# Performance work log

Measured on AMD Instinct MI355X. Metric: run time of the kernel, lower is better.

The kernel has to match this reference:

```python
import jax, jax.numpy as jnp
import numpy as np

H, DM, N, K, R = 768, 1536, 16, 4, 48  # hidden, intermediate, state, conv kernel, dt rank
B, L = 2, 1024


def _silu(x):
    return x * jax.nn.sigmoid(x)


def _causal_conv(x, w, b):
    # x: [B, D, L]; w: [D, K] depthwise; causal left-pad K-1 (matches causal_conv1d_fn)
    out = jax.lax.conv_general_dilated(
        x, w[:, None, :], window_strides=(1,), padding=[(K - 1, 0)],
        feature_group_count=w.shape[0], dimension_numbers=('NCH', 'OIH', 'NCH'))
    return out + b[None, :, None]


def _selective_scan(u, delta, A, Bm, Cm, Dp, gate):
    # u/delta/gate: [B, D, L]; A: [D, N]; Bm/Cm: [B, L, N]; Dp: [D]
    dA = jnp.exp(delta[:, :, :, None] * A[None, :, None, :])              # [B,D,L,N]
    dBu = delta[:, :, :, None] * Bm[:, None, :, :] * u[:, :, :, None]      # [B,D,L,N]
    dA_t = jnp.moveaxis(dA, 2, 0)    # [L,B,D,N]
    dBu_t = jnp.moveaxis(dBu, 2, 0)  # [L,B,D,N]
    C_t = jnp.moveaxis(Cm, 1, 0)     # [L,B,N]

    def step(x, inp):
        a, bu, c = inp
        x = a * x + bu                               # [B,D,N]
        y = jnp.einsum('bdn,bn->bd', x, c)
        return x, y

    x0 = jnp.zeros(dA_t.shape[1:], dA_t.dtype)
    _, ys = jax.lax.scan(step, x0, (dA_t, dBu_t, C_t))
    y = jnp.moveaxis(ys, 0, 2) + u * Dp[None, :, None]   # [B,D,L]
    return y * _silu(gate)


def _branch(conv_out, gate, xw, dtw, dtb, Alog, Dp):
    # conv_out/gate: [B, D, L]
    ssm = jnp.einsum('bdl,pd->blp', conv_out, xw)        # [B,L,R+2N]
    ts, Bm, Cm = ssm[..., :R], ssm[..., R:R + N], ssm[..., R + N:]
    delta = jax.nn.softplus(jnp.einsum('dr,blr->bdl', dtw, ts) + dtb[None, :, None])
    A = -jnp.exp(Alog)
    return _selective_scan(conv_out, delta, A, Bm, Cm, Dp, gate)


def setup_inputs() -> dict:
    key = jax.random.key(0)
    ks = jax.random.split(key, 12)
    s = 0.02
    hidden_states = jax.random.normal(ks[0], (B, L, H), jnp.float32)
    in_proj_w = jax.random.normal(ks[1], (2 * DM, H), jnp.float32) * s
    conv_w = jax.random.normal(ks[2], (DM, K), jnp.float32) * 0.3
    conv_b = jax.random.normal(ks[3], (DM,), jnp.float32) * s
    x_proj_w = jax.random.normal(ks[4], (R + 2 * N, DM), jnp.float32) * s
    dt_proj_w = jax.random.normal(ks[5], (DM, R), jnp.float32) * s
    dt_proj_b = -4.0 + 0.1 * jax.random.normal(ks[6], (DM,), jnp.float32)
    x_proj_back_w = jax.random.normal(ks[7], (R + 2 * N, DM), jnp.float32) * s
    dt_proj_back_w = jax.random.normal(ks[8], (DM, R), jnp.float32) * s
    dt_proj_back_b = -4.0 + 0.1 * jax.random.normal(ks[9], (DM,), jnp.float32)
    A_log = jnp.log(jnp.broadcast_to(jnp.arange(1, N + 1, dtype=jnp.float32)[None, :], (DM, N)))
    A_log_back = A_log
    D = jnp.ones((DM,), jnp.float32)
    D_back = jnp.ones((DM,), jnp.float32)
    out_proj_w = jax.random.normal(ks[10], (H, DM), jnp.float32) * s
    return {
        'hidden_states': hidden_states, 'in_proj_w': in_proj_w,
        'conv_w': conv_w, 'conv_b': conv_b,
        'x_proj_w': x_proj_w, 'dt_proj_w': dt_proj_w, 'dt_proj_b': dt_proj_b,
        'x_proj_back_w': x_proj_back_w, 'dt_proj_back_w': dt_proj_back_w,
        'dt_proj_back_b': dt_proj_back_b, 'A_log': A_log, 'A_log_back': A_log_back,
        'D': D, 'D_back': D_back, 'out_proj_w': out_proj_w,
    }


def reference(hidden_states, in_proj_w, conv_w, conv_b, x_proj_w, dt_proj_w,
              dt_proj_b, x_proj_back_w, dt_proj_back_w, dt_proj_back_b,
              A_log, A_log_back, D, D_back, out_proj_w):
    proj = jnp.einsum('blh,ph->bpl', hidden_states, in_proj_w)  # [B,2D,L]
    x, gate = proj[:, :DM], proj[:, DM:]
    conv_out = _silu(_causal_conv(x, conv_w, conv_b))           # [B,D,L]
    # forward-direction scan
    y_f = _branch(conv_out, gate, x_proj_w, dt_proj_w, dt_proj_b, A_log, D)
    # backward-direction scan on time-flipped conv output and gate
    y_b = _branch(conv_out[:, :, ::-1], gate[:, :, ::-1], x_proj_back_w,
                  dt_proj_back_w, dt_proj_back_b, A_log_back, D_back)
    y = y_f + y_b[:, :, ::-1]
    return jnp.einsum('bdl,hd->blh', y, out_proj_w)
```

## Files before the change

### kernel.cpp

```cpp
#include <hip/hip_runtime.h>
#include <math.h>

constexpr int cH  = 768;
constexpr int cDM = 1536;
constexpr int cN  = 16;
constexpr int cR  = 48;
constexpr int cB  = 2;
constexpr int cL  = 1024;
constexpr int cPS = 160;
constexpr int cCK = 32;

typedef unsigned short u16;
typedef __attribute__((ext_vector_type(8))) short bf16x8;
typedef __attribute__((ext_vector_type(4))) float f32x4;

__device__ __forceinline__ u16 f2bf(float f) {
    unsigned u = __float_as_uint(f);
    u += 0x7FFF + ((u >> 16) & 1);
    return (u16)(u >> 16);
}
__device__ __forceinline__ float bf2f(u16 h) {
    return __uint_as_float((unsigned)h << 16);
}
__device__ __forceinline__ float fexp2(float x) {
    float r; asm("v_exp_f32 %0, %1" : "=v"(r) : "v"(x)); return r;
}
constexpr float cLOG2E = 1.44269504f;

__global__ __launch_bounds__(256)
void prep_kernel(const float* __restrict__ hid, const float* __restrict__ inw,
                 const float* __restrict__ xpw, const float* __restrict__ xpbw,
                 const float* __restrict__ outw, const float* __restrict__ dtw,
                 const float* __restrict__ dtbw,
                 u16* __restrict__ hid_b, u16* __restrict__ inw_b,
                 u16* __restrict__ xpw2_b, u16* __restrict__ outw_b,
                 u16* __restrict__ dtw2_b)
{
    const long i8 = ((long)blockIdx.x * 256 + threadIdx.x) * 8;
    const long e0 = 1572864;
    const long e1 = e0 + 2359296;
    const long e2 = e1 + 122880;
    const long e3 = e2 + 122880;
    const long e4 = e3 + 1179648;
    const long e5 = e4 + 98304;
    const long e6 = e5 + 98304;
    const float* in; u16* out; long off; int pad = 0;
    if      (i8 < e0) { in = hid;  out = hid_b;           off = i8; }
    else if (i8 < e1) { in = inw;  out = inw_b;           off = i8 - e0; }
    else if (i8 < e2) { in = xpw;  out = xpw2_b;          off = i8 - e1; }
    else if (i8 < e3) { in = xpbw; out = xpw2_b + 122880; off = i8 - e2; }
    else if (i8 < e4) { in = outw; out = outw_b;          off = i8 - e3; }
    else if (i8 < e5) { in = dtw;  out = dtw2_b;          off = i8 - e4; pad = 1; }
    else if (i8 < e6) { in = dtbw; out = dtw2_b + 98304;  off = i8 - e5; pad = 1; }
    else return;
    u16 o[8];
    if (!pad) {
        const float4 a = *(const float4*)&in[off];
        const float4 b = *(const float4*)&in[off + 4];
        o[0]=f2bf(a.x); o[1]=f2bf(a.y); o[2]=f2bf(a.z); o[3]=f2bf(a.w);
        o[4]=f2bf(b.x); o[5]=f2bf(b.y); o[6]=f2bf(b.z); o[7]=f2bf(b.w);
    } else {
        const long r = off >> 6; const int k0 = (int)(off & 63);
        #pragma unroll
        for (int k = 0; k < 8; ++k)
            o[k] = (k0 + k < cR) ? f2bf(in[r * cR + k0 + k]) : (u16)0;
    }
    *(uint4*)&out[off] = *(uint4*)o;
}

__global__ __launch_bounds__(256)
void tspad_kernel(const float* __restrict__ ssms, u16* __restrict__ out) {
    int i = blockIdx.x * 256 + threadIdx.x;
    int dirsel = i >> 17;
    int rem = i & 131071;
    int bl = rem >> 6, k = rem & 63;
    out[i] = (k < cR) ? f2bf(ssms[(long)bl * cPS + dirsel * 80 + k]) : (u16)0;
}

__global__ __launch_bounds__(256)
void comb_kernel(u16* __restrict__ yf, const u16* __restrict__ yb, long n8) {
    long i = (long)blockIdx.x * 256 + threadIdx.x;
    if (i >= n8) return;
    uint4 av = ((uint4*)yf)[i];
    uint4 bv = ((const uint4*)yb)[i];
    unsigned* ap = (unsigned*)&av;
    unsigned* bp = (unsigned*)&bv;
    #pragma unroll
    for (int j = 0; j < 4; ++j) {
        const float lo = bf2f((u16)(ap[j] & 0xffff)) + bf2f((u16)(bp[j] & 0xffff));
        const float hi = bf2f((u16)(ap[j] >> 16))    + bf2f((u16)(bp[j] >> 16));
        ap[j] = (unsigned)f2bf(lo) | ((unsigned)f2bf(hi) << 16);
    }
    ((uint4*)yf)[i] = av;
}

__device__ __forceinline__ void gld_lds16(const u16* g, u16* l) {
    __builtin_amdgcn_global_load_lds(
        (const __attribute__((address_space(1))) unsigned int*)g,
        (__attribute__((address_space(3))) unsigned int*)l, 16, 0, 0);
}

#define GST(SA, SB, k0) do {                                                   \
    _Pragma("unroll")                                                          \
    for (int h = 0; h < 3; ++h) {                                              \
        const int q  = wid * 3 + h;                                            \
        const int rw = lane >> 2;                                              \
        if (q < 4) {                                                           \
            const int r  = q * 16 + rw;                                        \
            const int sw = (r & 3) ^ ((r >> 2) & 3);                           \
            const int kg = (k0) + (((lane & 3) ^ sw) << 3);                    \
            gld_lds16(Ab + (long)(m0 + r) * lda + kg, &SA[q * 512]);           \
        } else {                                                               \
            const int r  = (q - 4) * 16 + rw;                                  \
            const int sw = (r & 3) ^ ((r >> 2) & 3);                           \
            const int kg = (k0) + (((lane & 3) ^ sw) << 3);                    \
            int nr = n0 + r; if (nr > N2 - 1) nr = N2 - 1;                     \
            gld_lds16(Bb + (long)nr * ldb + kg, &SB[(q - 4) * 512]);           \
        }                                                                      \
    }                                                                          \
} while (0)

#define CMP(SA, SB) do {                                                       \
    bf16x8 af[4], bfr[2];                                                      \
    _Pragma("unroll")                                                          \
    for (int i = 0; i < 4; ++i) {                                              \
        const int ra  = i * 16 + lr;                                           \
        const int swa = (ra & 3) ^ ((ra >> 2) & 3);                            \
        af[i] = *(const bf16x8*)&SA[ra * 32 + ((lc ^ swa) << 3)];              \
    }                                                                          \
    _Pragma("unroll")                                                          \
    for (int j = 0; j < 2; ++j) {                                              \
        const int rb  = wn + j * 16 + lr;                                      \
        const int swb = (rb & 3) ^ ((rb >> 2) & 3);                            \
        bfr[j] = *(const bf16x8*)&SB[rb * 32 + ((lc ^ swb) << 3)];             \
    }                                                                          \
    _Pragma("unroll")                                                          \
    for (int i = 0; i < 4; ++i)                                                \
        _Pragma("unroll")                                                      \
        for (int j = 0; j < 2; ++j)                                            \
            acc[i][j] = __builtin_amdgcn_mfma_f32_16x16x32_bf16(af[i], bfr[j], acc[i][j], 0, 0, 0); \
} while (0)

template<int EPI>
__global__ __launch_bounds__(256, 4)
void gemm_mfma(const u16* __restrict__ A, const u16* __restrict__ B,
               float* __restrict__ C0, float* __restrict__ C1,
               const float* __restrict__ bias,
               int N2, int Kd, int lda, int ldb, int ldc,
               long sA, long sC, int splitCol, int kspl)
{
    __shared__ __align__(16) u16 shA0[2048];
    __shared__ __align__(16) u16 shA1[2048];
    __shared__ __align__(16) u16 shB0[4096];
    __shared__ __align__(16) u16 shB1[4096];
    const int tid  = threadIdx.x;
    const int wid  = tid >> 6, lane = tid & 63;
    const int lr   = lane & 15, lc = lane >> 4;
    const int z    = blockIdx.z;
    const int bz   = z / kspl, ks = z % kspl;
    const int kpc  = Kd / kspl;
    const int kbeg = ks * kpc;
    const int nt   = kpc / 32;
    const int n0 = blockIdx.x * 128, m0 = blockIdx.y * 64;
    const int wn = wid * 32;

    const u16* Ab = A + (long)bz * sA;
    const u16* Bb = B;

    f32x4 acc[4][2] = {};

    GST(shA0, shB0, kbeg);
    __syncthreads();
    int t = 0;
    for (;;) {
        if (t + 1 < nt) GST(shA1, shB1, kbeg + (t + 1) * 32);
        CMP(shA0, shB0);
        __syncthreads();
        if (++t >= nt) break;
        if (t + 1 < nt) GST(shA0, shB0, kbeg + (t + 1) * 32);
        CMP(shA1, shB1);
        __syncthreads();
        if (++t >= nt) break;
    }

    #pragma unroll
    for (int i = 0; i < 4; ++i) {
        #pragma unroll
        for (int e = 0; e < 4; ++e) {
            const int m = m0 + i * 16 + lc * 4 + e;
            float* base0 = C0 + (long)bz * sC + (long)m * ldc;
            float* base1 = (C1 != nullptr) ? C1 + (long)bz * sC + (long)m * ldc : nullptr;
            #pragma unroll
            for (int j = 0; j < 2; ++j) {
                const int n = n0 + wn + j * 16 + lr;
                if (n < N2) {
                    float v = acc[i][j][e];
                    if (EPI == 4) {
                        if (n < splitCol) base0[n] = v;
                        else base1[n - splitCol] = v / (1.f + __expf(-v));
                    } else if (EPI == 1) {
                        const float t2 = v + bias[n];
                        base0[n] = fmaxf(t2, 0.f) + __logf(1.f + __expf(-fabsf(t2)));
                    } else {
                        atomicAdd(base0 + n, v);
                    }
                }
            }
        }
    }
}

__global__ __launch_bounds__(256)
void conv_silu2(const float* __restrict__ x, const float* __restrict__ cw,
                const float* __restrict__ cb,
                float* __restrict__ convTf, u16* __restrict__ convT_b)
{
    __shared__ float xt[35][64];
    const int l0 = blockIdx.x * 32, d0 = blockIdx.y * 64, b = blockIdx.z;
    const int tid = threadIdx.x;
    for (int i = tid; i < 35 * 64; i += 256) {
        const int r = i >> 6, c = i & 63;
        const int l = l0 - 3 + r;
        xt[r][c] = (l >= 0) ? x[((long)b * cL + l) * cDM + d0 + c] : 0.f;
    }
    __syncthreads();
    const int dc = tid & 63, lsub = tid >> 6;
    const int d = d0 + dc;
    const float w0 = cw[d*4], w1 = cw[d*4+1], w2 = cw[d*4+2], w3 = cw[d*4+3];
    const float bi = cb[d];
    #pragma unroll
    for (int k = 0; k < 8; ++k) {
        const int row = lsub * 8 + k;
        float v = bi;
        v = fmaf(w0, xt[row][dc],     v);
        v = fmaf(w1, xt[row + 1][dc], v);
        v = fmaf(w2, xt[row + 2][dc], v);
        v = fmaf(w3, xt[row + 3][dc], v);
        const float s = v / (1.f + __expf(-v));
        const long o = ((long)b * cL + l0 + row) * cDM + d;
        convTf[o] = s;
        convT_b[o] = f2bf(s);
    }
}

#define SA_LOAD(g, DU, UU) _Pragma("unroll")                                   \
    for (int k = 0; k < 4; ++k) {                                              \
        const int t_ = (g) * 4 + k;                                            \
        const int l_ = dir ? (base - t_) : (base + t_);                        \
        const long off_ = (long)l_ * cDM + d;                                  \
        DU[k] = dT[off_]; UU[k] = uT[off_];                                    \
    }

#define SA_COMP(g, DU, UU) _Pragma("unroll")                                   \
    for (int k = 0; k < 4; ++k) {                                              \
        const int t_ = (g) * 4 + k;                                            \
        const float du_ = DU[k]; const float duu_ = du_ * UU[k];               \
        sdu += du_;                                                            \
        const float4 b0_ = *(const float4*)&bca[t_][half * 8];                 \
        const float4 b1_ = *(const float4*)&bca[t_][half * 8 + 4];             \
        const float bb_[8] = {b0_.x,b0_.y,b0_.z,b0_.w,b1_.x,b1_.y,b1_.z,b1_.w};\
        _Pragma("unroll")                                                      \
        for (int n = 0; n < 8; ++n)                                            \
            xs[n] = fmaf(fexp2(du_ * a2[n]), xs[n], duu_ * bb_[n]);            \
    }

__global__ __launch_bounds__(256, 4)
void scanA_kernel(const float* __restrict__ dT0, const float* __restrict__ dT1,
                  const float* __restrict__ uF, const float* __restrict__ ssms,
                  const float* __restrict__ AlogF, const float* __restrict__ AlogB,
                  float* __restrict__ Ap_out, float* __restrict__ Xf_out)
{
    __shared__ float bcA[4][32][16];
    const int tid = threadIdx.x;
    const int w = tid >> 6, lane = tid & 63;
    const int dd = lane & 31, half = lane >> 5;
    const int d = blockIdx.x * 32 + dd;
    const int b = blockIdx.y;
    const int zs = blockIdx.z * 4 + w;
    const int dir = zs >> 5, ck = zs & 31;
    const float* Alog = dir ? AlogB : AlogF;
    const float* dT = (dir ? dT1 : dT0) + (long)b * cL * cDM;
    const float* uT = uF + (long)b * cL * cDM;
    const float* sp = ssms + (long)b * cL * cPS;
    const int sofs = dir ? 128 : 48;
    const int base = dir ? (cL - 1 - ck * 32) : (ck * 32);
    float (*bca)[16] = bcA[w];

    #pragma unroll
    for (int h = 0; h < 2; ++h) {
        const int idx = h * 64 + lane;
        const int r = idx >> 2, q = idx & 3;
        const int lr_ = dir ? (base - r) : (base + r);
        *(float4*)&bca[r][q * 4] = *(const float4*)&sp[(long)lr_ * cPS + sofs + q * 4];
    }
    float a2[8];
    {
        const float4 a0 = *(const float4*)&Alog[d * 16 + half * 8];
        const float4 a1 = *(const float4*)&Alog[d * 16 + half * 8 + 4];
        a2[0]=-__expf(a0.x)*cLOG2E; a2[1]=-__expf(a0.y)*cLOG2E;
        a2[2]=-__expf(a0.z)*cLOG2E; a2[3]=-__expf(a0.w)*cLOG2E;
        a2[4]=-__expf(a1.x)*cLOG2E; a2[5]=-__expf(a1.y)*cLOG2E;
        a2[6]=-__expf(a1.z)*cLOG2E; a2[7]=-__expf(a1.w)*cLOG2E;
    }

    float xs[8] = {};
    float sdu = 0.f;

    float dX[4], uX[4], dY[4], uY[4], dZ[4], uZ[4];
    SA_LOAD(0, dX, uX);
    SA_LOAD(1, dY, uY);
    SA_LOAD(2, dZ, uZ);
    SA_COMP(0, dX, uX); SA_LOAD(3, dX, uX);
    SA_COMP(1, dY, uY); SA_LOAD(4, dY, uY);
    SA_COMP(2, dZ, uZ); SA_LOAD(5, dZ, uZ);
    SA_COMP(3, dX, uX); SA_LOAD(6, dX, uX);
    SA_COMP(4, dY, uY); SA_LOAD(7, dY, uY);
    SA_COMP(5, dZ, uZ);
    SA_COMP(6, dX, uX);
    SA_COMP(7, dY, uY);

    const long ob = (((long)(b * 2 + dir) * cCK + ck) * cDM + d) * 16 + half * 8;
    *(float4*)&Ap_out[ob]     = make_float4(fexp2(sdu*a2[0]), fexp2(sdu*a2[1]),
                                            fexp2(sdu*a2[2]), fexp2(sdu*a2[3]));
    *(float4*)&Ap_out[ob + 4] = make_float4(fexp2(sdu*a2[4]), fexp2(sdu*a2[5]),
                                            fexp2(sdu*a2[6]), fexp2(sdu*a2[7]));
    *(float4*)&Xf_out[ob]     = make_float4(xs[0], xs[1], xs[2], xs[3]);
    *(float4*)&Xf_out[ob + 4] = make_float4(xs[4], xs[5], xs[6], xs[7]);
}

__global__ __launch_bounds__(256)
void scanB_kernel(float* __restrict__ Ap, const float* __restrict__ Xf)
{
    const int gid = blockIdx.x * 256 + threadIdx.x;
    const int n = gid & 15;
    const int rest = gid >> 4;
    const int d = rest % cDM;
    const int b2 = rest / cDM;
    float x0 = 0.f;
    #pragma unroll
    for (int c = 0; c < cCK; ++c) {
        const long idx = (((long)b2 * cCK + c) * cDM + d) * 16 + n;
        const float ap = Ap[idx], xf = Xf[idx];
        Ap[idx] = x0;
        x0 = fmaf(ap, x0, xf);
    }
}

#define SC_LOAD(g, DU, UU, SG) _Pragma("unroll")                               \
    for (int k = 0; k < 4; ++k) {                                              \
        const int t_ = (g) * 4 + k;                                            \
        const int l_ = dir ? (base - t_) : (base + t_);                        \
        const long off_ = (long)l_ * cDM + d;                                  \
        DU[k] = dT[off_]; UU[k] = uT[off_];                                    \
        if (half == 0) SG[k] = sgp[off_];                                      \
    }

#define SC_COMP(g, DU, UU, SG) _Pragma("unroll")                               \
    for (int k = 0; k < 4; ++k) {                                              \
        const int t_ = (g) * 4 + k;                                            \
        const float du_ = DU[k]; const float uu_ = UU[k];                      \
        const float duu_ = du_ * uu_;                                          \
        const float4 b0_ = *(const float4*)&bcc[t_][half * 8];                 \
        const float4 b1_ = *(const float4*)&bcc[t_][half * 8 + 4];             \
        const float4 c0_ = *(const float4*)&bcc[t_][16 + half * 8];            \
        const float4 c1_ = *(const float4*)&bcc[t_][16 + half * 8 + 4];        \
        const float bb_[8] = {b0_.x,b0_.y,b0_.z,b0_.w,b1_.x,b1_.y,b1_.z,b1_.w};\
        const float cc_[8] = {c0_.x,c0_.y,c0_.z,c0_.w,c1_.x,c1_.y,c1_.z,c1_.w};\
        float y_ = 0.f;                                                        \
        _Pragma("unroll")                                                      \
        for (int n = 0; n < 8; ++n) {                                          \
            xs[n] = fmaf(fexp2(du_ * a2[n]), xs[n], duu_ * bb_[n]);            \
            y_ = fmaf(xs[n], cc_[n], y_);                                      \
        }                                                                      \
        y_ += __shfl_xor(y_, 32);                                              \
        if (half == 0) {                                                       \
            const int l2_ = dir ? (base - t_) : (base + t_);                   \
            const float val_ = (y_ + uu_ * Dd) * SG[k];                        \
            yout[((long)b * cL + l2_) * cDM + d] = f2bf(val_);                 \
        }                                                                      \
    }

__global__ __launch_bounds__(256, 4)
void scanC_kernel(const float* __restrict__ dT0, const float* __restrict__ dT1,
                  const float* __restrict__ uF, const float* __restrict__ sgF,
                  const float* __restrict__ ssms,
                  const float* __restrict__ AlogF, const float* __restrict__ AlogB,
                  const float* __restrict__ Df, const float* __restrict__ Db,
                  const float* __restrict__ X0,
                  u16* __restrict__ yf, u16* __restrict__ yb)
{
    __shared__ float bcS[4][32][32];
    const int tid = threadIdx.x;
    const int w = tid >> 6, lane = tid & 63;
    const int dd = lane & 31, half = lane >> 5;
    const int d = blockIdx.x * 32 + dd;
    const int b = blockIdx.y;
    const int zs = blockIdx.z * 4 + w;
    const int dir = zs >> 5, ck = zs & 31;
    const float* Alog = dir ? AlogB : AlogF;
    const float* dT = (dir ? dT1 : dT0) + (long)b * cL * cDM;
    const float* uT = uF + (long)b * cL * cDM;
    const float* sgp = sgF + (long)b * cL * cDM;
    const float* sp = ssms + (long)b * cL * cPS;
    const float Dd = dir ? Db[d] : Df[d];
    u16* yout = dir ? yb : yf;
    const int sofs = dir ? 128 : 48;
    const int base = dir ? (cL - 1 - ck * 32) : (ck * 32);
    float (*bcc)[32] = bcS[w];

    #pragma unroll
    for (int h = 0; h < 4; ++h) {
        const int idx = h * 64 + lane;
        const int r = idx >> 3, q = idx & 7;
        const int lr_ = dir ? (base - r) : (base + r);
        *(float4*)&bcc[r][q * 4] = *(const float4*)&sp[(long)lr_ * cPS + sofs + q * 4];
    }
    float a2[8];
    {
        const float4 a0 = *(const float4*)&Alog[d * 16 + half * 8];
        const float4 a1 = *(const float4*)&Alog[d * 16 + half * 8 + 4];
        a2[0]=-__expf(a0.x)*cLOG2E; a2[1]=-__expf(a0.y)*cLOG2E;
        a2[2]=-__expf(a0.z)*cLOG2E; a2[3]=-__expf(a0.w)*cLOG2E;
        a2[4]=-__expf(a1.x)*cLOG2E; a2[5]=-__expf(a1.y)*cLOG2E;
        a2[6]=-__expf(a1.z)*cLOG2E; a2[7]=-__expf(a1.w)*cLOG2E;
    }
    float xs[8];
    {
        const long ob = (((long)(b * 2 + dir) * cCK + ck) * cDM + d) * 16 + half * 8;
        const float4 x0v = *(const float4*)&X0[ob];
        const float4 x1v = *(const float4*)&X0[ob + 4];
        xs[0]=x0v.x; xs[1]=x0v.y; xs[2]=x0v.z; xs[3]=x0v.w;
        xs[4]=x1v.x; xs[5]=x1v.y; xs[6]=x1v.z; xs[7]=x1v.w;
    }

    float dX[4], uX[4], gX[4], dY[4], uY[4], gY[4], dZ[4], uZ[4], gZ[4];
    SC_LOAD(0, dX, uX, gX);
    SC_LOAD(1, dY, uY, gY);
    SC_LOAD(2, dZ, uZ, gZ);
    SC_COMP(0, dX, uX, gX); SC_LOAD(3, dX, uX, gX);
    SC_COMP(1, dY, uY, gY); SC_LOAD(4, dY, uY, gY);
    SC_COMP(2, dZ, uZ, gZ); SC_LOAD(5, dZ, uZ, gZ);
    SC_COMP(3, dX, uX, gX); SC_LOAD(6, dX, uX, gX);
    SC_COMP(4, dY, uY, gY); SC_LOAD(7, dY, uY, gY);
    SC_COMP(5, dZ, uZ, gZ);
    SC_COMP(6, dX, uX, gX);
    SC_COMP(7, dY, uY, gY);
}

extern "C" void kernel_launch(void* const* d_in, const int* in_sizes, int n_in,
                              void* d_out, int out_size, void* d_ws, size_t ws_size,
                              hipStream_t stream)
{
    const float* hid   = (const float*)d_in[0];
    const float* inw   = (const float*)d_in[1];
    const float* convw = (const float*)d_in[2];
    const float* convb = (const float*)d_in[3];
    const float* xpw   = (const float*)d_in[4];
    const float* dtw   = (const float*)d_in[5];
    const float* dtb   = (const float*)d_in[6];
    const float* xpbw  = (const float*)d_in[7];
    const float* dtbw  = (const float*)d_in[8];
    const float* dtbb  = (const float*)d_in[9];
    const float* Alog  = (const float*)d_in[10];
    const float* Alogb = (const float*)d_in[11];
    const float* Dv    = (const float*)d_in[12];
    const float* Dbv   = (const float*)d_in[13];
    const float* outw  = (const float*)d_in[14];
    float* out = (float*)d_out;

    float* ws = (float*)d_ws;
    const long S = (long)cB * cDM * cL;
    const long nSum = (long)2 * cB * cCK * cDM * 16;
    float* xbuf   = ws;
    float* sg     = ws + S;
    float* convTf = ws + 2 * S;
    float* deltaT1= ws + 3 * S;
    float* ssms   = ws + 4 * S;
    float* sumAp  = ssms + (long)cB * cL * cPS;
    float* sumXf  = sumAp + nSum;
    u16* ub       = (u16*)(sumXf + nSum);
    u16* convT_b  = ub;
    u16* yf_b     = convT_b + S;
    u16* yb_b     = yf_b + S;
    u16* ts2_b    = yb_b + S;
    u16* xpw2_b   = ts2_b + (long)2 * cB * cL * 64;
    u16* dtw2_b   = xpw2_b + (long)cPS * cDM;
    u16* outw_b   = dtw2_b + (long)2 * cDM * 64;
    u16* inw_b    = outw_b + (long)cH * cDM;
    u16* hid_b    = inw_b + (long)2 * cDM * cH;

    const dim3 blk(256);

    prep_kernel<<<dim3(2713), blk, 0, stream>>>(
        hid, inw, xpw, xpbw, outw, dtw, dtbw,
        hid_b, inw_b, xpw2_b, outw_b, dtw2_b);

    hipMemsetAsync(ssms, 0, (long)cB * cL * cPS * sizeof(float), stream);
    hipMemsetAsync(out, 0, (long)out_size * sizeof(float), stream);

    gemm_mfma<4><<<dim3(24, 16, cB), blk, 0, stream>>>(
        hid_b, inw_b, xbuf, sg, nullptr,
        2 * cDM, cH, cH, cH, cDM, (long)cL * cH, (long)cL * cDM, cDM, 1);

    conv_silu2<<<dim3(32, 24, cB), blk, 0, stream>>>(
        xbuf, convw, convb, convTf, convT_b);

    gemm_mfma<2><<<dim3(2, 16, cB * 8), blk, 0, stream>>>(
        convT_b, xpw2_b, ssms, nullptr, nullptr,
        cPS, cDM, cDM, cDM, cPS, (long)cL * cDM, (long)cL * cPS, 1 << 30, 8);

    tspad_kernel<<<1024, blk, 0, stream>>>(ssms, ts2_b);

    gemm_mfma<1><<<dim3(12, 16, cB), blk, 0, stream>>>(
        ts2_b, dtw2_b, xbuf, nullptr, dtb,
        cDM, 64, 64, 64, cDM, (long)cL * 64, (long)cL * cDM, 1 << 30, 1);
    gemm_mfma<1><<<dim3(12, 16, cB), blk, 0, stream>>>(
        ts2_b + (long)2 * cL * 64, dtw2_b + (long)cDM * 64, deltaT1, nullptr, dtbb,
        cDM, 64, 64, 64, cDM, (long)cL * 64, (long)cL * cDM, 1 << 30, 1);

    scanA_kernel<<<dim3(48, cB, 16), blk, 0, stream>>>(
        xbuf, deltaT1, convTf, ssms, Alog, Alogb, sumAp, sumXf);
    scanB_kernel<<<dim3(384), blk, 0, stream>>>(sumAp, sumXf);
    scanC_kernel<<<dim3(48, cB, 16), blk, 0, stream>>>(
        xbuf, deltaT1, convTf, sg, ssms, Alog, Alogb, Dv, Dbv,
        sumAp , yf_b, yb_b);

    comb_kernel<<<(int)(S / 8 / 256), blk, 0, stream>>>(yf_b, yb_b, S / 8);

    gemm_mfma<2><<<dim3(6, 16, cB * 2), blk, 0, stream>>>(
        yf_b, outw_b, out, nullptr, nullptr,
        cH, cDM, cDM, cDM, cH, (long)cL * cDM, (long)cL * cH, 1 << 30, 2);
}
```

Baseline: 169.1 us.

## Split scan kernels into single-wave blocks and store chunk delta sums instead of decay products

The scanA and scanC kernels are relaunched with one 64-thread wave per block instead of four waves sharing a block, which gives finer scheduling granularity and adds a __syncthreads after the shared B/C staging. ScanA now writes only the per-chunk sum of delta per channel rather than 16 exponentiated decay products, and scanB recomputes exp2(A*sum) itself. This cuts scanA output traffic, and scanB now writes the carried prefix state in place into the Xf buffer. The compute loops are also wrapped in s_setprio raises so the arithmetic phases get wave priority over loads.

```diff
diff --git a/kernel.cpp b/kernel.cpp
--- a/kernel.cpp
+++ b/kernel.cpp
@@ -251,47 +251,49 @@
         DU[k] = dT[off_]; UU[k] = uT[off_];                                    \
     }
 
-#define SA_COMP(g, DU, UU) _Pragma("unroll")                                   \
+#define SA_COMP(g, DU, UU) do {                                                \
+    __builtin_amdgcn_s_setprio(1);                                             \
+    _Pragma("unroll")                                                          \
     for (int k = 0; k < 4; ++k) {                                              \
         const int t_ = (g) * 4 + k;                                            \
         const float du_ = DU[k]; const float duu_ = du_ * UU[k];               \
         sdu += du_;                                                            \
-        const float4 b0_ = *(const float4*)&bca[t_][half * 8];                 \
-        const float4 b1_ = *(const float4*)&bca[t_][half * 8 + 4];             \
+        const float4 b0_ = *(const float4*)&bcA[t_][half * 8];                 \
+        const float4 b1_ = *(const float4*)&bcA[t_][half * 8 + 4];             \
         const float bb_[8] = {b0_.x,b0_.y,b0_.z,b0_.w,b1_.x,b1_.y,b1_.z,b1_.w};\
         _Pragma("unroll")                                                      \
         for (int n = 0; n < 8; ++n)                                            \
             xs[n] = fmaf(fexp2(du_ * a2[n]), xs[n], duu_ * bb_[n]);            \
-    }
-
-__global__ __launch_bounds__(256, 4)
+    }                                                                          \
+    __builtin_amdgcn_s_setprio(0);                                             \
+} while (0)
+
+__global__ __launch_bounds__(64, 4)
 void scanA_kernel(const float* __restrict__ dT0, const float* __restrict__ dT1,
                   const float* __restrict__ uF, const float* __restrict__ ssms,
                   const float* __restrict__ AlogF, const float* __restrict__ AlogB,
-                  float* __restrict__ Ap_out, float* __restrict__ Xf_out)
-{
-    __shared__ float bcA[4][32][16];
-    const int tid = threadIdx.x;
-    const int w = tid >> 6, lane = tid & 63;
+                  float* __restrict__ sdu_out, float* __restrict__ Xf_out)
+{
+    __shared__ float bcA[32][16];
+    const int lane = threadIdx.x;
     const int dd = lane & 31, half = lane >> 5;
     const int d = blockIdx.x * 32 + dd;
     const int b = blockIdx.y;
-    const int zs = blockIdx.z * 4 + w;
-    const int dir = zs >> 5, ck = zs & 31;
+    const int z = blockIdx.z;
+    const int dir = z >> 5, ck = z & 31;
     const float* Alog = dir ? AlogB : AlogF;
     const float* dT = (dir ? dT1 : dT0) + (long)b * cL * cDM;
     const float* uT = uF + (long)b * cL * cDM;
     const float* sp = ssms + (long)b * cL * cPS;
     const int sofs = dir ? 128 : 48;
     const int base = dir ? (cL - 1 - ck * 32) : (ck * 32);
-    float (*bca)[16] = bcA[w];
 
     #pragma unroll
     for (int h = 0; h < 2; ++h) {
         const int idx = h * 64 + lane;
         const int r = idx >> 2, q = idx & 3;
         const int lr_ = dir ? (base - r) : (base + r);
-        *(float4*)&bca[r][q * 4] = *(const float4*)&sp[(long)lr_ * cPS + sofs + q * 4];
+        *(float4*)&bcA[r][q * 4] = *(const float4*)&sp[(long)lr_ * cPS + sofs + q * 4];
     }
     float a2[8];
     {
@@ -302,6 +304,7 @@
         a2[4]=-__expf(a1.x)*cLOG2E; a2[5]=-__expf(a1.y)*cLOG2E;
         a2[6]=-__expf(a1.z)*cLOG2E; a2[7]=-__expf(a1.w)*cLOG2E;
     }
+    __syncthreads();
 
     float xs[8] = {};
     float sdu = 0.f;
@@ -319,29 +322,33 @@
     SA_COMP(6, dX, uX);
     SA_COMP(7, dY, uY);
 
+    if (half == 0)
+        sdu_out[((long)(b * 2 + dir) * cCK + ck) * cDM + d] = sdu;
     const long ob = (((long)(b * 2 + dir) * cCK + ck) * cDM + d) * 16 + half * 8;
-    *(float4*)&Ap_out[ob]     = make_float4(fexp2(sdu*a2[0]), fexp2(sdu*a2[1]),
-                                            fexp2(sdu*a2[2]), fexp2(sdu*a2[3]));
-    *(float4*)&Ap_out[ob + 4] = make_float4(fexp2(sdu*a2[4]), fexp2(sdu*a2[5]),
-                                            fexp2(sdu*a2[6]), fexp2(sdu*a2[7]));
     *(float4*)&Xf_out[ob]     = make_float4(xs[0], xs[1], xs[2], xs[3]);
     *(float4*)&Xf_out[ob + 4] = make_float4(xs[4], xs[5], xs[6], xs[7]);
 }
 
 __global__ __launch_bounds__(256)
-void scanB_kernel(float* __restrict__ Ap, const float* __restrict__ Xf)
+void scanB_kernel(const float* __restrict__ AlogF, const float* __restrict__ AlogB,
+                  const float* __restrict__ sduB, float* __restrict__ Xf)
 {
     const int gid = blockIdx.x * 256 + threadIdx.x;
     const int n = gid & 15;
     const int rest = gid >> 4;
     const int d = rest % cDM;
     const int b2 = rest / cDM;
+    const int dir = b2 & 1;
+    const float* Alog = dir ? AlogB : AlogF;
+    const float a2 = -__expf(Alog[d * 16 + n]) * cLOG2E;
     float x0 = 0.f;
     #pragma unroll
     for (int c = 0; c < cCK; ++c) {
-        const long idx = (((long)b2 * cCK + c) * cDM + d) * 16 + n;
-        const float ap = Ap[idx], xf = Xf[idx];
-        Ap[idx] = x0;
+        const long sidx = ((long)b2 * cCK + c) * cDM + d;
+        const float ap = fexp2(a2 * sduB[sidx]);
+        const long idx = sidx * 16 + n;
+        const float xf = Xf[idx];
+        Xf[idx] = x0;
         x0 = fmaf(ap, x0, xf);
     }
 }
@@ -355,15 +362,17 @@
         if (half == 0) SG[k] = sgp[off_];                                      \
     }
 
-#define SC_COMP(g, DU, UU, SG) _Pragma("unroll")                               \
+#define SC_COMP(g, DU, UU, SG) do {                                            \
+    __builtin_amdgcn_s_setprio(1);                                             \
+    _Pragma("unroll")                                                          \
     for (int k = 0; k < 4; ++k) {                                              \
         const int t_ = (g) * 4 + k;                                            \
         const float du_ = DU[k]; const float uu_ = UU[k];                      \
         const float duu_ = du_ * uu_;                                          \
-        const float4 b0_ = *(const float4*)&bcc[t_][half * 8];                 \
-        const float4 b1_ = *(const float4*)&bcc[t_][half * 8 + 4];             \
-        const float4 c0_ = *(const float4*)&bcc[t_][16 + half * 8];            \
-        const float4 c1_ = *(const float4*)&bcc[t_][16 + half * 8 + 4];        \
+        const float4 b0_ = *(const float4*)&bc[t_][half * 8];                  \
+        const float4 b1_ = *(const float4*)&bc[t_][half * 8 + 4];              \
+        const float4 c0_ = *(const float4*)&bc[t_][16 + half * 8];             \
+        const float4 c1_ = *(const float4*)&bc[t_][16 + half * 8 + 4];         \
         const float bb_[8] = {b0_.x,b0_.y,b0_.z,b0_.w,b1_.x,b1_.y,b1_.z,b1_.w};\
         const float cc_[8] = {c0_.x,c0_.y,c0_.z,c0_.w,c1_.x,c1_.y,c1_.z,c1_.w};\
         float y_ = 0.f;                                                        \
@@ -378,9 +387,11 @@
             const float val_ = (y_ + uu_ * Dd) * SG[k];                        \
             yout[((long)b * cL + l2_) * cDM + d] = f2bf(val_);                 \
         }                                                                      \
-    }
-
-__global__ __launch_bounds__(256, 4)
+    }                                                                          \
+    __builtin_amdgcn_s_setprio(0);                                             \
+} while (0)
+
+__global__ __launch_bounds__(64, 4)
 void scanC_kernel(const float* __restrict__ dT0, const float* __restrict__ dT1,
                   const float* __restrict__ uF, const float* __restrict__ sgF,
                   const float* __restrict__ ssms,
@@ -389,14 +400,13 @@
                   const float* __restrict__ X0,
                   u16* __restrict__ yf, u16* __restrict__ yb)
 {
-    __shared__ float bcS[4][32][32];
-    const int tid = threadIdx.x;
-    const int w = tid >> 6, lane = tid & 63;
+    __shared__ float bc[32][32];
+    const int lane = threadIdx.x;
     const int dd = lane & 31, half = lane >> 5;
     const int d = blockIdx.x * 32 + dd;
     const int b = blockIdx.y;
-    const int zs = blockIdx.z * 4 + w;
-    const int dir = zs >> 5, ck = zs & 31;
+    const int z = blockIdx.z;
+    const int dir = z >> 5, ck = z & 31;
     const float* Alog = dir ? AlogB : AlogF;
     const float* dT = (dir ? dT1 : dT0) + (long)b * cL * cDM;
     const float* uT = uF + (long)b * cL * cDM;
@@ -406,14 +416,13 @@
     u16* yout = dir ? yb : yf;
     const int sofs = dir ? 128 : 48;
     const int base = dir ? (cL - 1 - ck * 32) : (ck * 32);
-    float (*bcc)[32] = bcS[w];
 
     #pragma unroll
     for (int h = 0; h < 4; ++h) {
         const int idx = h * 64 + lane;
         const int r = idx >> 3, q = idx & 7;
         const int lr_ = dir ? (base - r) : (base + r);
-        *(float4*)&bcc[r][q * 4] = *(const float4*)&sp[(long)lr_ * cPS + sofs + q * 4];
+        *(float4*)&bc[r][q * 4] = *(const float4*)&sp[(long)lr_ * cPS + sofs + q * 4];
     }
     float a2[8];
     {
@@ -432,6 +441,7 @@
         xs[0]=x0v.x; xs[1]=x0v.y; xs[2]=x0v.z; xs[3]=x0v.w;
         xs[4]=x1v.x; xs[5]=x1v.y; xs[6]=x1v.z; xs[7]=x1v.w;
     }
+    __syncthreads();
 
     float dX[4], uX[4], gX[4], dY[4], uY[4], gY[4], dZ[4], uZ[4], gZ[4];
     SC_LOAD(0, dX, uX, gX);
@@ -471,14 +481,15 @@
     float* ws = (float*)d_ws;
     const long S = (long)cB * cDM * cL;
     const long nSum = (long)2 * cB * cCK * cDM * 16;
+    const long nSdu = (long)2 * cB * cCK * cDM;
     float* xbuf   = ws;
     float* sg     = ws + S;
     float* convTf = ws + 2 * S;
     float* deltaT1= ws + 3 * S;
     float* ssms   = ws + 4 * S;
-    float* sumAp  = ssms + (long)cB * cL * cPS;
-    float* sumXf  = sumAp + nSum;
-    u16* ub       = (u16*)(sumXf + nSum);
+    float* sumXf  = ssms + (long)cB * cL * cPS;
+    float* sduBuf = sumXf + nSum;
+    u16* ub       = (u16*)(sduBuf + nSdu);
     u16* convT_b  = ub;
     u16* yf_b     = convT_b + S;
     u16* yb_b     = yf_b + S;
@@ -518,12 +529,12 @@
         ts2_b + (long)2 * cL * 64, dtw2_b + (long)cDM * 64, deltaT1, nullptr, dtbb,
         cDM, 64, 64, 64, cDM, (long)cL * 64, (long)cL * cDM, 1 << 30, 1);
 
-    scanA_kernel<<<dim3(48, cB, 16), blk, 0, stream>>>(
-        xbuf, deltaT1, convTf, ssms, Alog, Alogb, sumAp, sumXf);
-    scanB_kernel<<<dim3(384), blk, 0, stream>>>(sumAp, sumXf);
-    scanC_kernel<<<dim3(48, cB, 16), blk, 0, stream>>>(
+    scanA_kernel<<<dim3(48, cB, 64), dim3(64), 0, stream>>>(
+        xbuf, deltaT1, convTf, ssms, Alog, Alogb, sduBuf, sumXf);
+    scanB_kernel<<<dim3(384), blk, 0, stream>>>(Alog, Alogb, sduBuf, sumXf);
+    scanC_kernel<<<dim3(48, cB, 64), dim3(64), 0, stream>>>(
         xbuf, deltaT1, convTf, sg, ssms, Alog, Alogb, Dv, Dbv,
-        sumAp , yf_b, yb_b);
+        sumXf , yf_b, yb_b);
 
     comb_kernel<<<(int)(S / 8 / 256), blk, 0, stream>>>(yf_b, yb_b, S / 8);
 
```

Measured after the change: 577.8 us. 242% more time.
